# Kernel optimization log

Measured on AMD Instinct MI355X. Metric: run time of the kernel, lower is better.

The kernel has to match this reference:

```python
import jax, jax.numpy as jnp
import numpy as np
from jax.ops import segment_sum

N_NODES = 100000
N_EDGES = 1600000


def _add_self_loops(edge_index, n):
    loop = jnp.arange(n, dtype=edge_index.dtype)
    src = jnp.concatenate([edge_index[0], loop])
    dst = jnp.concatenate([edge_index[1], loop])
    return src, dst


def _gcn_norm(src, dst, n):
    # symmetric normalization deg^{-1/2}[src] * deg^{-1/2}[dst], degrees on dst
    deg = segment_sum(jnp.ones_like(dst, dtype=jnp.float32), dst, num_segments=n)
    dinv = jnp.where(deg > 0, jax.lax.rsqrt(deg), 0.0)
    return dinv[src] * dinv[dst]


def _gcn_conv(x, W, b, src, dst, norm, n):
    xw = x @ W                      # [N, out]
    msg = xw[src] * norm[:, None]   # gather + scale, [E+N, out]
    out = segment_sum(msg, dst, num_segments=n)  # scatter-add
    return out + b


def setup_inputs() -> dict:
    key = jax.random.key(0)
    ks = jax.random.split(key, 8)
    x = jax.random.normal(ks[0], (N_NODES, 165), dtype=jnp.float32)
    edge_index = jax.random.randint(ks[1], (2, N_EDGES), 0, N_NODES, dtype=jnp.int64)
    W1 = jax.random.normal(ks[2], (165, 128), dtype=jnp.float32) / np.sqrt(165.0)
    b1 = jnp.zeros((128,), dtype=jnp.float32)
    W2 = jax.random.normal(ks[3], (128, 2), dtype=jnp.float32) / np.sqrt(128.0)
    b2 = jnp.zeros((2,), dtype=jnp.float32)
    Wc = jax.random.normal(ks[4], (2, 1), dtype=jnp.float32) / np.sqrt(2.0)
    bc = jnp.zeros((1,), dtype=jnp.float32)
    return {"x": x, "edge_index": edge_index, "W1": W1, "b1": b1,
            "W2": W2, "b2": b2, "Wc": Wc, "bc": bc}


def reference(x, edge_index, W1, b1, W2, b2, Wc, bc):
    n = x.shape[0]
    src, dst = _add_self_loops(edge_index, n)
    norm = _gcn_norm(src, dst, n)
    h = _gcn_conv(x, W1, b1, src, dst, norm, n)
    h = jax.nn.relu(h)              # dropout is identity in eval mode
    h = _gcn_conv(h, W2, b2, src, dst, norm, n)
    h = jax.nn.relu(h)
    out = h @ Wc + bc
    return jax.nn.sigmoid(out)
```

## Files before the change

### kernel.cpp

```cpp
#include <hip/hip_runtime.h>
#include <hip/hip_fp16.h>
#include <stdint.h>

#define NN 100000
#define NB 512
#define BUCKET 196
#define BPAD 4096
#define TILE 4096
#define EPT 16

typedef _Float16 f16x8 __attribute__((ext_vector_type(8)));
typedef float f32x4  __attribute__((ext_vector_type(4)));

__device__ __forceinline__ __half2 u2h(unsigned u){ return *(__half2*)&u; }

__global__ __launch_bounds__(256) void k_init(const void* __restrict__ ep, int* __restrict__ flag,
                                              long long E, long long nn,
                                              const float* __restrict__ W1, _Float16* __restrict__ Bf,
                                              int* __restrict__ cnt){
    int b = blockIdx.x, t = threadIdx.x;
    if (b == 0){
        __shared__ int bad;
        if (t == 0) bad = 0;
        __syncthreads();
        const long long* p = (const long long*)ep;
        for (long long i = t; i < 1024 && i < E; i += 256){
            long long v = p[i];
            if (v < 0 || v >= nn) atomicOr(&bad, 1);
        }
        __syncthreads();
        if (t == 0) flag[0] = bad ? 0 : 1;
        cnt[t] = 0; cnt[t + 256] = 0;
    } else {
        int q = (b - 1) * 256 + t;
        int k = q >> 7, c = q & 127;
        float w = (k < 165) ? W1[k * 128 + c] : 0.0f;
        int tt = k >> 5, kk = k & 31;
        int lane = ((kk >> 3) << 4) + (c & 15);
        int j = kk & 7;
        int fq = c >> 4;
        Bf[(((tt * 8 + fq) * 64 + lane) << 3) + j] = (_Float16)w;
    }
}

__global__ __launch_bounds__(256) void k_scatter(const void* __restrict__ ep, const int* __restrict__ flag,
                                                 int* __restrict__ cnt, unsigned* __restrict__ rec, int E){
    __shared__ int h[NB];
    __shared__ int gb[NB];
    __shared__ int lo[NB];
    __shared__ int sc[256];
    __shared__ unsigned staged[TILE];
    __shared__ int sdst[TILE];
    int t = threadIdx.x;
    int f = flag[0];
    long long base = (long long)blockIdx.x * TILE;
    for (int i = t; i < NB; i += 256) h[i] = 0;
    __syncthreads();

    int s[EPT], dl[EPT], r[EPT], bb[EPT];
    if (f){
        const long long* p = (const long long*)ep;
        #pragma unroll
        for (int ch = 0; ch < 8; ++ch){
            long long e = base + ((long long)(ch * 256 + t)) * 2;
            int j0 = 2 * ch, j1 = j0 + 1;
            if (e + 1 < E){
                longlong2 sv = *(const longlong2*)(p + e);
                longlong2 dv = *(const longlong2*)(p + E + e);
                s[j0] = (int)sv.x; s[j1] = (int)sv.y;
                int d0 = (int)dv.x, d1 = (int)dv.y;
                bb[j0] = d0 / BUCKET; dl[j0] = d0 - bb[j0] * BUCKET;
                bb[j1] = d1 / BUCKET; dl[j1] = d1 - bb[j1] * BUCKET;
            } else {
                bb[j0] = -1; bb[j1] = -1;
                if (e < E){
                    s[j0] = (int)p[e];
                    int d0 = (int)p[E + e];
                    bb[j0] = d0 / BUCKET; dl[j0] = d0 - bb[j0] * BUCKET;
                }
            }
        }
    } else {
        const int* p = (const int*)ep;
        #pragma unroll
        for (int ch = 0; ch < 4; ++ch){
            long long e = base + ((long long)(ch * 256 + t)) * 4;
            int j0 = 4 * ch;
            if (e + 3 < E){
                int4 sv = *(const int4*)(p + e);
                int4 dv = *(const int4*)(p + E + e);
                int ss[4] = {sv.x, sv.y, sv.z, sv.w};
                int dd[4] = {dv.x, dv.y, dv.z, dv.w};
                #pragma unroll
                for (int q = 0; q < 4; ++q){
                    s[j0 + q] = ss[q];
                    bb[j0 + q] = dd[q] / BUCKET;
                    dl[j0 + q] = dd[q] - bb[j0 + q] * BUCKET;
                }
            } else {
                #pragma unroll
                for (int q = 0; q < 4; ++q){
                    bb[j0 + q] = -1;
                    if (e + q < E){
                        s[j0 + q] = p[e + q];
                        int d = p[E + e + q];
                        bb[j0 + q] = d / BUCKET;
                        dl[j0 + q] = d - bb[j0 + q] * BUCKET;
                    }
                }
            }
        }
    }
    #pragma unroll
    for (int j = 0; j < EPT; ++j)
        if (bb[j] >= 0) r[j] = atomicAdd(&h[bb[j]], 1);
    __syncthreads();

    {
        int b0 = 2 * t, b1i = b0 + 1;
        int own = h[b0] + h[b1i];
        sc[t] = own; __syncthreads();
        for (int off = 1; off < 256; off <<= 1){
            int u = (t >= off) ? sc[t - off] : 0;
            __syncthreads();
            sc[t] += u;
            __syncthreads();
        }
        int excl = sc[t] - own;
        lo[b0]  = excl;
        lo[b1i] = excl + h[b0];
    }
    for (int i = t; i < NB; i += 256)
        gb[i] = h[i] ? (i * BPAD + atomicAdd(&cnt[i], h[i])) : 0;
    __syncthreads();
    #pragma unroll
    for (int j = 0; j < EPT; ++j){
        if (bb[j] >= 0){
            int slot = lo[bb[j]] + r[j];
            staged[slot] = ((unsigned)dl[j] << 24) | (unsigned)s[j];
            int dstpos = gb[bb[j]] + r[j];
            sdst[slot] = (dstpos < bb[j] * BPAD + BPAD) ? dstpos : -1;
        }
    }
    __syncthreads();
    long long cntE64 = E - base;
    int cntE = (cntE64 < TILE) ? (int)cntE64 : TILE;
    for (int q = t; q < cntE; q += 256)
        if (sdst[q] >= 0) rec[sdst[q]] = staged[q];
}

__global__ __launch_bounds__(256) void k_csr(const unsigned* __restrict__ rec, const int* __restrict__ cnt,
                                             int* __restrict__ rp, int* __restrict__ rpe, int* __restrict__ col,
                                             float* __restrict__ dinv){
    int b = blockIdx.x;
    int t = threadIdx.x;
    int d0 = b * BUCKET;
    if (d0 >= NN) return;
    int e0 = b * BPAD;
    int e1 = e0 + cnt[b];
    __shared__ int h[BUCKET];
    __shared__ int sc[256];
    __shared__ int cur[BUCKET];
    for (int i = t; i < BUCKET; i += 256) h[i] = 0;
    __syncthreads();
    for (int e = e0 + t; e < e1; e += 256)
        atomicAdd(&h[rec[e] >> 24], 1);
    __syncthreads();
    int own = (t < BUCKET) ? h[t] : 0;
    sc[t] = own; __syncthreads();
    for (int off = 1; off < 256; off <<= 1){
        int u = (t >= off) ? sc[t - off] : 0;
        __syncthreads();
        sc[t] += u;
        __syncthreads();
    }
    int excl = sc[t] - own;
    if (t < BUCKET && d0 + t < NN){
        rp[d0 + t]   = e0 + excl;
        rpe[d0 + t]  = e0 + excl + own;
        cur[t]       = e0 + excl;
        dinv[d0 + t] = rsqrtf((float)(own + 1));
    }
    __syncthreads();
    for (int e = e0 + t; e < e1; e += 256){
        unsigned v = rec[e];
        int p = atomicAdd(&cur[v >> 24], 1);
        col[p] = (int)(v & 0xFFFFFFu);
    }
}

#define GSTRIDE 200
#define GCSTR   136
__global__ __launch_bounds__(64) void k_gemm1(const float* __restrict__ x,
                                              const _Float16* __restrict__ Bf16,
                                              const float* __restrict__ dinv,
                                              _Float16* __restrict__ xws, int n){
    __shared__ _Float16 As[16 * GSTRIDE];
    int lane = threadIdx.x;
    int i0 = blockIdx.x * 16;

    for (int q = lane; q < 16 * 27; q += 64){
        int r = q / 27, k = 165 + (q - r * 27);
        As[r * GSTRIDE + k] = (_Float16)0.0f;
    }

    {
        const float4* src4 = (const float4*)(x + (size_t)i0 * 165);
        float4 v[11];
        #pragma unroll
        for (int u = 0; u < 10; ++u)
            v[u] = src4[lane + u * 64];
        v[10] = (lane < 20) ? src4[lane + 640] : make_float4(0, 0, 0, 0);
        #pragma unroll
        for (int u = 0; u < 11; ++u){
            if (u == 10 && lane >= 20) break;
            int e0i = (lane + u * 64) * 4;
            int r = e0i / 165;
            int k = e0i - r * 165;
            float c[4] = {v[u].x, v[u].y, v[u].z, v[u].w};
            #pragma unroll
            for (int cc = 0; cc < 4; ++cc){
                As[r * GSTRIDE + k] = (_Float16)c[cc];
                if (++k == 165){ k = 0; ++r; }
            }
        }
    }
    __syncthreads();

    int rl = lane & 15, kg = lane >> 4;
    f32x4 acc[8];
    #pragma unroll
    for (int cf = 0; cf < 8; ++cf) acc[cf] = (f32x4)0.0f;

    #pragma unroll
    for (int tt = 0; tt < 6; ++tt){
        f16x8 a = *(const f16x8*)&As[rl * GSTRIDE + tt * 32 + kg * 8];
        #pragma unroll
        for (int cf = 0; cf < 8; ++cf){
            f16x8 b = *(const f16x8*)&Bf16[((tt * 8 + cf) * 64 + lane) << 3];
            acc[cf] = __builtin_amdgcn_mfma_f32_16x16x32_f16(a, b, acc[cf], 0, 0, 0);
        }
    }
    __syncthreads();

    _Float16* Cs = (_Float16*)As;
    float dv[4];
    #pragma unroll
    for (int r = 0; r < 4; ++r){
        int row = i0 + kg * 4 + r;
        dv[r] = (row < n) ? dinv[row] : 0.0f;
    }
    #pragma unroll
    for (int cf = 0; cf < 8; ++cf)
        #pragma unroll
        for (int r = 0; r < 4; ++r)
            Cs[(kg * 4 + r) * GCSTR + cf * 16 + rl] = (_Float16)(acc[cf][r] * dv[r]);
    __syncthreads();
    #pragma unroll
    for (int q = 0; q < 4; ++q){
        int idx = q * 64 + lane;
        int row = idx >> 4, cw = idx & 15;
        if (i0 + row < n){
            uint4 vv = *(const uint4*)&Cs[row * GCSTR + cw * 8];
            *(uint4*)&xws[((size_t)(i0 + row)) * 128 + cw * 8] = vv;
        }
    }
}

__global__ __launch_bounds__(256) void k_spmm1(const uint2* __restrict__ xg, const int* __restrict__ rp,
                                               const int* __restrict__ rpe, const int* __restrict__ col,
                                               const float* __restrict__ dinv,
                                               const float* __restrict__ b1, const float* __restrict__ W2,
                                               float* __restrict__ hw2s, int n){
    int i = (blockIdx.x * 256 + threadIdx.x) >> 6;
    int lane = threadIdx.x & 63;
    if (i >= n) return;
    int e0 = rp[i], e1 = rpe[i];
    float di = dinv[i];
    int lf = lane & 31;
    int hi = lane >> 5;
    __half2 a0 = __float2half2_rn(0.0f), a1 = a0;
    if (lane < 32){
        uint2 v = xg[(size_t)i * 32 + lf];
        a0 = u2h(v.x); a1 = u2h(v.y);
    }
    int e = e0;
    for (; e + 16 <= e1; e += 16){
        int c = col[e + lane];
        #pragma unroll
        for (int k = 0; k < 8; ++k){
            int sL = __builtin_amdgcn_readlane(c, 2 * k);
            int sH = __builtin_amdgcn_readlane(c, 2 * k + 1);
            int s = hi ? sH : sL;
            uint2 v = xg[(size_t)s * 32 + lf];
            a0 = __hadd2(a0, u2h(v.x));
            a1 = __hadd2(a1, u2h(v.y));
        }
    }
    int rem = e1 - e;
    if (rem > 0){
        int c = (lane < rem) ? col[e + lane] : 0;
        int kmax = (rem + 1) >> 1;
        #pragma unroll
        for (int k = 0; k < 8; ++k){
            if (k < kmax){
                int sL = __builtin_amdgcn_readlane(c, 2 * k);
                int sH = __builtin_amdgcn_readlane(c, 2 * k + 1);
                int s = hi ? sH : sL;
                uint2 v = xg[(size_t)s * 32 + lf];
                if (2 * k + hi < rem){
                    a0 = __hadd2(a0, u2h(v.x));
                    a1 = __hadd2(a1, u2h(v.y));
                }
            }
        }
    }
    {
        int u0 = __shfl_xor(*(int*)&a0, 32);
        int u1 = __shfl_xor(*(int*)&a1, 32);
        a0 = __hadd2(a0, u2h((unsigned)u0));
        a1 = __hadd2(a1, u2h((unsigned)u1));
    }
    int f0 = 4 * lf;
    float4 bv = *(const float4*)(b1 + f0);
    float h0 = fmaxf(di * __low2float(a0)  + bv.x, 0.0f);
    float h1 = fmaxf(di * __high2float(a0) + bv.y, 0.0f);
    float h2 = fmaxf(di * __low2float(a1)  + bv.z, 0.0f);
    float h3 = fmaxf(di * __high2float(a1) + bv.w, 0.0f);
    float4 w01 = *(const float4*)(W2 + 2 * f0);
    float4 w23 = *(const float4*)(W2 + 2 * f0 + 4);
    float s0 = h0 * w01.x + h1 * w01.z + h2 * w23.x + h3 * w23.z;
    float s1 = h0 * w01.y + h1 * w01.w + h2 * w23.y + h3 * w23.w;
    #pragma unroll
    for (int off = 1; off < 32; off <<= 1){
        s0 += __shfl_xor(s0, off);
        s1 += __shfl_xor(s1, off);
    }
    if (lane == 0)
        *(float2*)(hw2s + 2 * i) = make_float2(s0 * di, s1 * di);
}

__global__ __launch_bounds__(256) void k_spmm2(const int* __restrict__ rp, const int* __restrict__ rpe,
                                               const int* __restrict__ col,
                                               const float* __restrict__ dinv, const float* __restrict__ hw2s,
                                               const float* __restrict__ b2, const float* __restrict__ Wc,
                                               const float* __restrict__ bc, float* __restrict__ out, int n){
    int wave = threadIdx.x >> 6, lane = threadIdx.x & 63;
    int g = lane >> 3, j = lane & 7;
    int node = blockIdx.x * 32 + wave * 8 + g;
    if (node >= n) return;
    int e0 = rp[node], e1 = rpe[node];
    float s0 = 0.0f, s1 = 0.0f;
    if (j == 0){ s0 = hw2s[2 * node]; s1 = hw2s[2 * node + 1]; }
    for (int e = e0 + j; e < e1; e += 8){
        int c = col[e];
        float2 v = *(const float2*)(hw2s + 2 * c);
        s0 += v.x; s1 += v.y;
    }
    #pragma unroll
    for (int off = 1; off < 8; off <<= 1){
        s0 += __shfl_xor(s0, off);
        s1 += __shfl_xor(s1, off);
    }
    if (j == 0){
        float di = dinv[node];
        float a0 = fmaxf(di * s0 + b2[0], 0.0f);
        float a1 = fmaxf(di * s1 + b2[1], 0.0f);
        float z = a0 * Wc[0] + a1 * Wc[1] + bc[0];
        out[node] = 1.0f / (1.0f + expf(-z));
    }
}

extern "C" void kernel_launch(void* const* d_in, const int* in_sizes, int n_in,
                              void* d_out, int out_size, void* d_ws, size_t ws_size,
                              hipStream_t stream) {
    const float* x  = (const float*)d_in[0];
    const void*  ei = d_in[1];
    const float* W1 = (const float*)d_in[2];
    const float* b1 = (const float*)d_in[3];
    const float* W2 = (const float*)d_in[4];
    const float* b2 = (const float*)d_in[5];
    const float* Wc = (const float*)d_in[6];
    const float* bc = (const float*)d_in[7];
    float* out = (float*)d_out;

    const int n = NN;
    const int E = in_sizes[1] / 2;

    char* ws = (char*)d_ws;
    size_t off = 0;
    auto alloc = [&](size_t bytes)->char*{
        off = (off + 255) & ~(size_t)255;
        char* p = ws + off; off += bytes; return p;
    };
    int*      flag    = (int*)alloc(4);
    int*      cnt     = (int*)alloc((size_t)NB * 4);
    int*      rp      = (int*)alloc((size_t)n * 4);
    int*      rpe     = (int*)alloc((size_t)n * 4);
    float*    dinv    = (float*)alloc((size_t)n * 4);
    float*    hw2s    = (float*)alloc((size_t)n * 2 * 4);
    _Float16* Bf      = (_Float16*)alloc((size_t)192 * 128 * 2);
    int*      col     = (int*)alloc((size_t)NB * BPAD * 4);
    unsigned* rec     = (unsigned*)alloc((size_t)NB * BPAD * 4);
    _Float16* xws;
    {
        size_t xws_bytes = (size_t)n * 128 * 2;
        size_t off_sep = (off + 255) & ~(size_t)255;
        if (off_sep + xws_bytes <= ws_size) xws = (_Float16*)alloc(xws_bytes);
        else                                xws = (_Float16*)rec;
    }
    (void)n_in; (void)out_size;

    int gT = (E + TILE - 1) / TILE;
    int gS1 = (n + 3) / 4;
    int gS2 = (n + 31) / 32;

    k_init<<<97, 256, 0, stream>>>(ei, flag, (long long)E, (long long)n, W1, Bf, cnt);
    k_scatter<<<gT, 256, 0, stream>>>(ei, flag, cnt, rec, E);
    k_csr<<<NB, 256, 0, stream>>>(rec, cnt, rp, rpe, col, dinv);
    k_gemm1<<<(n + 15) / 16, 64, 0, stream>>>(x, Bf, dinv, xws, n);
    k_spmm1<<<gS1, 256, 0, stream>>>((const uint2*)xws, rp, rpe, col, dinv, b1, W2, hw2s, n);
    k_spmm2<<<gS2, 256, 0, stream>>>(rp, rpe, col, dinv, hw2s, b2, Wc, bc, out, n);
}
```

Before: 142.0 us.

## Store layer-1 projected features as FP8 and gather four edges per wave

```diff
diff --git a/kernel.cpp b/kernel.cpp
--- a/kernel.cpp
+++ b/kernel.cpp
@@ -11,8 +11,7 @@
 
 typedef _Float16 f16x8 __attribute__((ext_vector_type(8)));
 typedef float f32x4  __attribute__((ext_vector_type(4)));
-
-__device__ __forceinline__ __half2 u2h(unsigned u){ return *(__half2*)&u; }
+typedef float f32x2  __attribute__((ext_vector_type(2)));
 
 __global__ __launch_bounds__(256) void k_init(const void* __restrict__ ep, int* __restrict__ flag,
                                               long long E, long long nn,
@@ -190,11 +189,11 @@
 }
 
 #define GSTRIDE 200
-#define GCSTR   136
+#define CSTR8   144
 __global__ __launch_bounds__(64) void k_gemm1(const float* __restrict__ x,
                                               const _Float16* __restrict__ Bf16,
                                               const float* __restrict__ dinv,
-                                              _Float16* __restrict__ xws, int n){
+                                              unsigned char* __restrict__ xws, int n){
     __shared__ _Float16 As[16 * GSTRIDE];
     int lane = threadIdx.x;
     int i0 = blockIdx.x * 16;
@@ -243,7 +242,7 @@
     }
     __syncthreads();
 
-    _Float16* Cs = (_Float16*)As;
+    unsigned char* Cs = (unsigned char*)As;
     float dv[4];
     #pragma unroll
     for (int r = 0; r < 4; ++r){
@@ -253,21 +252,24 @@
     #pragma unroll
     for (int cf = 0; cf < 8; ++cf)
         #pragma unroll
-        for (int r = 0; r < 4; ++r)
-            Cs[(kg * 4 + r) * GCSTR + cf * 16 + rl] = (_Float16)(acc[cf][r] * dv[r]);
-    __syncthreads();
-    #pragma unroll
-    for (int q = 0; q < 4; ++q){
+        for (int r = 0; r < 4; ++r){
+            float v = acc[cf][r] * dv[r];
+            int p = __builtin_amdgcn_cvt_pk_fp8_f32(v, v, 0, false);
+            Cs[(kg * 4 + r) * CSTR8 + cf * 16 + rl] = (unsigned char)(p & 0xFF);
+        }
+    __syncthreads();
+    #pragma unroll
+    for (int q = 0; q < 2; ++q){
         int idx = q * 64 + lane;
-        int row = idx >> 4, cw = idx & 15;
+        int row = idx >> 3, cw = idx & 7;
         if (i0 + row < n){
-            uint4 vv = *(const uint4*)&Cs[row * GCSTR + cw * 8];
-            *(uint4*)&xws[((size_t)(i0 + row)) * 128 + cw * 8] = vv;
-        }
-    }
-}
-
-__global__ __launch_bounds__(256) void k_spmm1(const uint2* __restrict__ xg, const int* __restrict__ rp,
+            uint4 vv = *(const uint4*)&Cs[row * CSTR8 + cw * 16];
+            *(uint4*)&xws[((size_t)(i0 + row)) * 128 + cw * 16] = vv;
+        }
+    }
+}
+
+__global__ __launch_bounds__(256) void k_spmm1(const unsigned char* __restrict__ xb, const int* __restrict__ rp,
                                                const int* __restrict__ rpe, const int* __restrict__ col,
                                                const float* __restrict__ dinv,
                                                const float* __restrict__ b1, const float* __restrict__ W2,
@@ -277,62 +279,77 @@
     if (i >= n) return;
     int e0 = rp[i], e1 = rpe[i];
     float di = dinv[i];
-    int lf = lane & 31;
-    int hi = lane >> 5;
-    __half2 a0 = __float2half2_rn(0.0f), a1 = a0;
-    if (lane < 32){
-        uint2 v = xg[(size_t)i * 32 + lf];
-        a0 = u2h(v.x); a1 = u2h(v.y);
+    int lf8 = lane & 15;
+    int eg  = lane >> 4;
+    f32x2 A0 = 0.0f, A1 = 0.0f, A2 = 0.0f, A3 = 0.0f;
+    if (lane < 16){
+        uint2 v = *(const uint2*)(xb + ((size_t)i << 7) + (lf8 << 3));
+        A0 += __builtin_amdgcn_cvt_pk_f32_fp8(v.x, false);
+        A1 += __builtin_amdgcn_cvt_pk_f32_fp8(v.x, true);
+        A2 += __builtin_amdgcn_cvt_pk_f32_fp8(v.y, false);
+        A3 += __builtin_amdgcn_cvt_pk_f32_fp8(v.y, true);
     }
     int e = e0;
     for (; e + 16 <= e1; e += 16){
         int c = col[e + lane];
         #pragma unroll
-        for (int k = 0; k < 8; ++k){
-            int sL = __builtin_amdgcn_readlane(c, 2 * k);
-            int sH = __builtin_amdgcn_readlane(c, 2 * k + 1);
-            int s = hi ? sH : sL;
-            uint2 v = xg[(size_t)s * 32 + lf];
-            a0 = __hadd2(a0, u2h(v.x));
-            a1 = __hadd2(a1, u2h(v.y));
+        for (int k = 0; k < 4; ++k){
+            int s = __shfl(c, 4 * k + eg);
+            uint2 v = *(const uint2*)(xb + ((size_t)s << 7) + (lf8 << 3));
+            A0 += __builtin_amdgcn_cvt_pk_f32_fp8(v.x, false);
+            A1 += __builtin_amdgcn_cvt_pk_f32_fp8(v.x, true);
+            A2 += __builtin_amdgcn_cvt_pk_f32_fp8(v.y, false);
+            A3 += __builtin_amdgcn_cvt_pk_f32_fp8(v.y, true);
         }
     }
     int rem = e1 - e;
     if (rem > 0){
         int c = (lane < rem) ? col[e + lane] : 0;
-        int kmax = (rem + 1) >> 1;
-        #pragma unroll
-        for (int k = 0; k < 8; ++k){
+        int kmax = (rem + 3) >> 2;
+        #pragma unroll
+        for (int k = 0; k < 4; ++k){
             if (k < kmax){
-                int sL = __builtin_amdgcn_readlane(c, 2 * k);
-                int sH = __builtin_amdgcn_readlane(c, 2 * k + 1);
-                int s = hi ? sH : sL;
-                uint2 v = xg[(size_t)s * 32 + lf];
-                if (2 * k + hi < rem){
-                    a0 = __hadd2(a0, u2h(v.x));
-                    a1 = __hadd2(a1, u2h(v.y));
+                int s = __shfl(c, 4 * k + eg);
+                uint2 v = *(const uint2*)(xb + ((size_t)s << 7) + (lf8 << 3));
+                if (4 * k + eg < rem){
+                    A0 += __builtin_amdgcn_cvt_pk_f32_fp8(v.x, false);
+                    A1 += __builtin_amdgcn_cvt_pk_f32_fp8(v.x, true);
+                    A2 += __builtin_amdgcn_cvt_pk_f32_fp8(v.y, false);
+                    A3 += __builtin_amdgcn_cvt_pk_f32_fp8(v.y, true);
                 }
             }
         }
     }
-    {
-        int u0 = __shfl_xor(*(int*)&a0, 32);
-        int u1 = __shfl_xor(*(int*)&a1, 32);
-        a0 = __hadd2(a0, u2h((unsigned)u0));
-        a1 = __hadd2(a1, u2h((unsigned)u1));
-    }
-    int f0 = 4 * lf;
-    float4 bv = *(const float4*)(b1 + f0);
-    float h0 = fmaxf(di * __low2float(a0)  + bv.x, 0.0f);
-    float h1 = fmaxf(di * __high2float(a0) + bv.y, 0.0f);
-    float h2 = fmaxf(di * __low2float(a1)  + bv.z, 0.0f);
-    float h3 = fmaxf(di * __high2float(a1) + bv.w, 0.0f);
-    float4 w01 = *(const float4*)(W2 + 2 * f0);
-    float4 w23 = *(const float4*)(W2 + 2 * f0 + 4);
-    float s0 = h0 * w01.x + h1 * w01.z + h2 * w23.x + h3 * w23.z;
-    float s1 = h0 * w01.y + h1 * w01.w + h2 * w23.y + h3 * w23.w;
-    #pragma unroll
-    for (int off = 1; off < 32; off <<= 1){
+    #pragma unroll
+    for (int off = 16; off < 64; off <<= 1){
+        f32x2 t0, t1, t2, t3;
+        t0.x = __shfl_xor(A0.x, off); t0.y = __shfl_xor(A0.y, off);
+        t1.x = __shfl_xor(A1.x, off); t1.y = __shfl_xor(A1.y, off);
+        t2.x = __shfl_xor(A2.x, off); t2.y = __shfl_xor(A2.y, off);
+        t3.x = __shfl_xor(A3.x, off); t3.y = __shfl_xor(A3.y, off);
+        A0 += t0; A1 += t1; A2 += t2; A3 += t3;
+    }
+    int f0 = 8 * lf8;
+    float4 bva = *(const float4*)(b1 + f0);
+    float4 bvb = *(const float4*)(b1 + f0 + 4);
+    float h0 = fmaxf(di * A0.x + bva.x, 0.0f);
+    float h1 = fmaxf(di * A0.y + bva.y, 0.0f);
+    float h2 = fmaxf(di * A1.x + bva.z, 0.0f);
+    float h3 = fmaxf(di * A1.y + bva.w, 0.0f);
+    float h4 = fmaxf(di * A2.x + bvb.x, 0.0f);
+    float h5 = fmaxf(di * A2.y + bvb.y, 0.0f);
+    float h6 = fmaxf(di * A3.x + bvb.z, 0.0f);
+    float h7 = fmaxf(di * A3.y + bvb.w, 0.0f);
+    float4 w0 = *(const float4*)(W2 + 2 * f0);
+    float4 w1 = *(const float4*)(W2 + 2 * f0 + 4);
+    float4 w2 = *(const float4*)(W2 + 2 * f0 + 8);
+    float4 w3 = *(const float4*)(W2 + 2 * f0 + 12);
+    float s0 = h0 * w0.x + h1 * w0.z + h2 * w1.x + h3 * w1.z
+             + h4 * w2.x + h5 * w2.z + h6 * w3.x + h7 * w3.z;
+    float s1 = h0 * w0.y + h1 * w0.w + h2 * w1.y + h3 * w1.w
+             + h4 * w2.y + h5 * w2.w + h6 * w3.y + h7 * w3.w;
+    #pragma unroll
+    for (int off = 1; off < 16; off <<= 1){
         s0 += __shfl_xor(s0, off);
         s1 += __shfl_xor(s1, off);
     }
@@ -402,12 +419,12 @@
     _Float16* Bf      = (_Float16*)alloc((size_t)192 * 128 * 2);
     int*      col     = (int*)alloc((size_t)NB * BPAD * 4);
     unsigned* rec     = (unsigned*)alloc((size_t)NB * BPAD * 4);
-    _Float16* xws;
+    unsigned char* xws;
     {
-        size_t xws_bytes = (size_t)n * 128 * 2;
+        size_t xws_bytes = (size_t)n * 128;
         size_t off_sep = (off + 255) & ~(size_t)255;
-        if (off_sep + xws_bytes <= ws_size) xws = (_Float16*)alloc(xws_bytes);
-        else                                xws = (_Float16*)rec;
+        if (off_sep + xws_bytes <= ws_size) xws = (unsigned char*)alloc(xws_bytes);
+        else                                xws = (unsigned char*)rec;
     }
     (void)n_in; (void)out_size;
 
@@ -419,6 +436,6 @@
     k_scatter<<<gT, 256, 0, stream>>>(ei, flag, cnt, rec, E);
     k_csr<<<NB, 256, 0, stream>>>(rec, cnt, rp, rpe, col, dinv);
     k_gemm1<<<(n + 15) / 16, 64, 0, stream>>>(x, Bf, dinv, xws, n);
-    k_spmm1<<<gS1, 256, 0, stream>>>((const uint2*)xws, rp, rpe, col, dinv, b1, W2, hw2s, n);
+    k_spmm1<<<gS1, 256, 0, stream>>>(xws, rp, rpe, col, dinv, b1, W2, hw2s, n);
     k_spmm2<<<gS2, 256, 0, stream>>>(rp, rpe, col, dinv, hw2s, b2, Wc, bc, out, n);
 }
```

New measurement: 131.1 us. 7.7% less time.
